# Optimization experiments

Hardware: AMD Instinct MI355X
Metric: run time of the kernel (lower is better)

Reference implementation:

```python
import jax, jax.numpy as jnp
import numpy as np

D = 128   # embedding_dim
H = 256   # hidden_dim

def setup_inputs() -> dict:
    key = jax.random.key(0)
    ks = jax.random.split(key, 16)
    s = 0.02
    B, N = 4, 384
    inp = {
        "cities": jax.random.uniform(ks[0], (B, N, 2), dtype=jnp.float32),
        # city_encoder: Linear(2,H) -> ReLU -> Linear(H,D); weights stored [in,out]
        "We1": jax.random.normal(ks[1], (2, H), dtype=jnp.float32) * s,
        "be1": jnp.zeros((H,), jnp.float32),
        "We2": jax.random.normal(ks[2], (H, D), dtype=jnp.float32) * s,
        "be2": jnp.zeros((D,), jnp.float32),
        # attention: Linear(D,H) -> ReLU -> Linear(H,1)
        "Wa1": jax.random.normal(ks[3], (D, H), dtype=jnp.float32) * s,
        "ba1": jnp.zeros((H,), jnp.float32),
        "wa2": jax.random.normal(ks[4], (H, 1), dtype=jnp.float32) * s,
        "ba2": jnp.zeros((1,), jnp.float32),
        # decoder: Linear(2D,H) -> ReLU -> Linear(H,1) -> Sigmoid
        "Wd1": jax.random.normal(ks[5], (2 * D, H), dtype=jnp.float32) * s,
        "bd1": jnp.zeros((H,), jnp.float32),
        "wd2": jax.random.normal(ks[6], (H, 1), dtype=jnp.float32) * s,
        "bd2": jnp.zeros((1,), jnp.float32),
    }
    return inp


def reference(cities, We1, be1, We2, be2, Wa1, ba1, wa2, ba2, Wd1, bd1, wd2, bd2):
    B, N, _ = cities.shape
    # city encoder MLP: [B,N,2] -> [B,N,D]
    emb = jax.nn.relu(cities @ We1 + be1) @ We2 + be2
    # attention scores -> softmax over cities
    att = jax.nn.softmax((jax.nn.relu(emb @ Wa1 + ba1) @ wa2 + ba2).squeeze(-1), axis=1)
    # Pairwise decoder: concat(e_i, e_j) @ Wd1 == e_i @ Wd1[:D] + e_j @ Wd1[D:]
    Ai = emb @ Wd1[:D]   # [B,N,H] contribution of row city i
    Aj = emb @ Wd1[D:]   # [B,N,H] contribution of col city j
    h = jax.nn.relu(Ai[:, :, None, :] + Aj[:, None, :, :] + bd1)  # [B,N,N,H]
    p = jax.nn.sigmoid((h @ wd2).squeeze(-1) + bd2)               # [B,N,N]
    # diagonal (i == j) was never written in the torch loop -> stays 0
    p = p * (1.0 - jnp.eye(N, dtype=p.dtype))
    return att, p
```

## Files before the change

### kernel.cpp

```cpp
#include <hip/hip_runtime.h>
#include <hip/hip_fp16.h>

#define NCITY 384
#define BATCH 4
#define DIM   128
#define HID   256
#define M_TOT (BATCH * NCITY)
#define TR    6

__device__ __forceinline__ void chunk_stream(
    const float* __restrict__ W,
    const float (*emb_s)[DIM], float* scr, int tid, float out6[TR])
{
    const int c4 = tid & 63;
    const int wv = tid >> 6;
    const int k0 = wv * 32;

    float4 acc[TR];
    #pragma unroll
    for (int rr = 0; rr < TR; ++rr) acc[rr] = make_float4(0.f, 0.f, 0.f, 0.f);

    #pragma unroll 2
    for (int kb = 0; kb < 32; kb += 4) {
        float4 ev[TR];
        #pragma unroll
        for (int rr = 0; rr < TR; ++rr)
            ev[rr] = *(const float4*)&emb_s[rr][k0 + kb];
        #pragma unroll
        for (int kk = 0; kk < 4; ++kk) {
            const float4 w4 = *(const float4*)&W[(k0 + kb + kk) * HID + c4 * 4];
            #pragma unroll
            for (int rr = 0; rr < TR; ++rr) {
                const float e = ((const float*)&ev[rr])[kk];
                acc[rr].x = fmaf(e, w4.x, acc[rr].x);
                acc[rr].y = fmaf(e, w4.y, acc[rr].y);
                acc[rr].z = fmaf(e, w4.z, acc[rr].z);
                acc[rr].w = fmaf(e, w4.w, acc[rr].w);
            }
        }
    }
    __syncthreads();
    #pragma unroll
    for (int rr = 0; rr < TR; ++rr)
        *(float4*)&scr[(wv * TR + rr) * HID + c4 * 4] = acc[rr];
    __syncthreads();
    #pragma unroll
    for (int rr = 0; rr < TR; ++rr)
        out6[rr] = scr[(0 * TR + rr) * HID + tid] + scr[(1 * TR + rr) * HID + tid]
                 + scr[(2 * TR + rr) * HID + tid] + scr[(3 * TR + rr) * HID + tid];
}

__global__ __launch_bounds__(256, 3) void encoder_stream(
    const float* __restrict__ cities,
    const float* __restrict__ We1, const float* __restrict__ be1,
    const float* __restrict__ We2, const float* __restrict__ be2,
    const float* __restrict__ Wa1, const float* __restrict__ ba1,
    const float* __restrict__ wa2, const float* __restrict__ ba2,
    const float* __restrict__ Wd1, const float* __restrict__ bd1,
    float* __restrict__ score, float* __restrict__ Ai, float* __restrict__ Aj)
{
    __shared__ float h1_s[TR][HID];
    __shared__ float emb_s[TR][DIM];
    __shared__ float scr[4 * TR * HID];
    __shared__ float red2[4][TR];

    const int tid = threadIdx.x;
    const int r0  = blockIdx.x * TR;

    {
        const float w0 = We1[tid], w1 = We1[HID + tid], b1v = be1[tid];
        #pragma unroll
        for (int rr = 0; rr < TR; ++rr) {
            const float cxx = cities[(r0 + rr) * 2];
            const float cyy = cities[(r0 + rr) * 2 + 1];
            h1_s[rr][tid] = fmaxf(fmaf(cxx, w0, fmaf(cyy, w1, b1v)), 0.f);
        }
    }
    __syncthreads();

    {
        const int d4 = tid & 31;
        const int k0 = (tid >> 5) * 32;
        float4 acc[TR];
        #pragma unroll
        for (int rr = 0; rr < TR; ++rr) acc[rr] = make_float4(0.f, 0.f, 0.f, 0.f);

        #pragma unroll 2
        for (int kb = 0; kb < 32; kb += 4) {
            float4 hv[TR];
            #pragma unroll
            for (int rr = 0; rr < TR; ++rr)
                hv[rr] = *(const float4*)&h1_s[rr][k0 + kb];
            #pragma unroll
            for (int kk = 0; kk < 4; ++kk) {
                const float4 w4 = *(const float4*)&We2[(k0 + kb + kk) * DIM + d4 * 4];
                #pragma unroll
                for (int rr = 0; rr < TR; ++rr) {
                    const float h = ((const float*)&hv[rr])[kk];
                    acc[rr].x = fmaf(h, w4.x, acc[rr].x);
                    acc[rr].y = fmaf(h, w4.y, acc[rr].y);
                    acc[rr].z = fmaf(h, w4.z, acc[rr].z);
                    acc[rr].w = fmaf(h, w4.w, acc[rr].w);
                }
            }
        }
        #pragma unroll
        for (int rr = 0; rr < TR; ++rr) {
            acc[rr].x += __shfl_xor(acc[rr].x, 32);
            acc[rr].y += __shfl_xor(acc[rr].y, 32);
            acc[rr].z += __shfl_xor(acc[rr].z, 32);
            acc[rr].w += __shfl_xor(acc[rr].w, 32);
        }
        if ((tid & 63) < 32) {
            const int wv = tid >> 6;
            #pragma unroll
            for (int rr = 0; rr < TR; ++rr)
                *(float4*)&scr[(wv * TR + rr) * DIM + d4 * 4] = acc[rr];
        }
        __syncthreads();
        for (int o = tid; o < TR * DIM; o += 256) {
            const int rr = o >> 7, d = o & (DIM - 1);
            emb_s[rr][d] = scr[(0 * TR + rr) * DIM + d] + scr[(1 * TR + rr) * DIM + d]
                         + scr[(2 * TR + rr) * DIM + d] + scr[(3 * TR + rr) * DIM + d]
                         + be2[d];
        }
        __syncthreads();
    }

    float o6[TR];

    chunk_stream(Wa1, emb_s, scr, tid, o6);
    {
        const float ba1v = ba1[tid], wa2v = wa2[tid];
        const int wv = tid >> 6;
        #pragma unroll
        for (int rr = 0; rr < TR; ++rr) {
            float v = fmaxf(o6[rr] + ba1v, 0.f) * wa2v;
            #pragma unroll
            for (int off = 32; off > 0; off >>= 1)
                v += __shfl_down(v, off);
            if ((tid & 63) == 0) red2[wv][rr] = v;
        }
        __syncthreads();
        if (tid < TR)
            score[r0 + tid] = red2[0][tid] + red2[1][tid] + red2[2][tid] + red2[3][tid];
    }

    chunk_stream(Wd1, emb_s, scr, tid, o6);
    {
        const float bd1v = bd1[tid];
        #pragma unroll
        for (int rr = 0; rr < TR; ++rr)
            Ai[(r0 + rr) * HID + tid] = o6[rr] + bd1v;
    }

    chunk_stream(Wd1 + DIM * HID, emb_s, scr, tid, o6);
    #pragma unroll
    for (int rr = 0; rr < TR; ++rr)
        Aj[(r0 + rr) * HID + tid] = o6[rr];
    (void)ba2;
}

__device__ __forceinline__ unsigned pk_add(unsigned a, unsigned b) {
    unsigned r; asm("v_pk_add_f16 %0, %1, %2" : "=v"(r) : "v"(a), "v"(b)); return r;
}
__device__ __forceinline__ unsigned pk_max0(unsigned a) {
    unsigned r; asm("v_pk_max_f16 %0, %1, %2" : "=v"(r) : "v"(a), "v"(0u)); return r;
}
__device__ __forceinline__ unsigned pk_fma(unsigned a, unsigned b, unsigned c) {
    unsigned r; asm("v_pk_fma_f16 %0, %1, %2, %3" : "=v"(r) : "v"(a), "v"(b), "v"(c)); return r;
}
__device__ __forceinline__ unsigned pack2(float a, float b) {
    union { __half2 h2; unsigned u; } c;
    c.h2 = __float22half2_rn(make_float2(a, b));
    return c.u;
}
__device__ __forceinline__ float sum2(unsigned u) {
    union { unsigned u; __half2 h2; } c; c.u = u;
    return __low2float(c.h2) + __high2float(c.h2);
}
union H8 { float4 f4; unsigned u[4]; };

__global__ __launch_bounds__(256) void pair_sm_kernel(
    const float* __restrict__ Ai, const float* __restrict__ Aj,
    const float* __restrict__ wd2, const float* __restrict__ bd2,
    const float* __restrict__ score, float* __restrict__ att,
    float* __restrict__ p)
{
    const int tid = threadIdx.x;
    const int b   = blockIdx.y;

    if (blockIdx.x == 144) {
        __shared__ float red[8];
        const int t = tid;
        const float v0 = score[b * NCITY + t];
        const bool  h2v = (t < NCITY - 256);
        const float v1 = h2v ? score[b * NCITY + 256 + t] : -3.4e38f;
        float m = fmaxf(v0, v1);
        #pragma unroll
        for (int off = 32; off > 0; off >>= 1)
            m = fmaxf(m, __shfl_down(m, off));
        if ((t & 63) == 0) red[t >> 6] = m;
        __syncthreads();
        m = fmaxf(fmaxf(red[0], red[1]), fmaxf(red[2], red[3]));
        const float e0 = __expf(v0 - m);
        const float e1 = h2v ? __expf(v1 - m) : 0.f;
        float s = e0 + e1;
        #pragma unroll
        for (int off = 32; off > 0; off >>= 1)
            s += __shfl_down(s, off);
        if ((t & 63) == 0) red[4 + (t >> 6)] = s;
        __syncthreads();
        s = red[4] + red[5] + red[6] + red[7];
        att[b * NCITY + t] = e0 / s;
        if (h2v) att[b * NCITY + 256 + t] = e1 / s;
        return;
    }

    __shared__ __half ai_s[32 * HID];
    __shared__ __half aj_s[32 * HID];
    __shared__ unsigned wd2h[HID / 2];

    const int i0 = (blockIdx.x / 12) * 32;
    const int j0 = (blockIdx.x % 12) * 32;

    if (tid < HID / 2) {
        const float2 w2 = *(const float2*)&wd2[tid * 2];
        wd2h[tid] = pack2(w2.x, w2.y);
    }

    for (int u = tid; u < 32 * 32; u += 256) {
        const int r = u >> 5, s = u & 31;
        const int su = (s ^ (r & 15)) * 8;
        {
            const int g = (b * NCITY + i0 + r) * HID + s * 8;
            const float4 f0 = *(const float4*)&Ai[g];
            const float4 f1 = *(const float4*)&Ai[g + 4];
            H8 pk;
            pk.u[0] = pack2(f0.x, f0.y);
            pk.u[1] = pack2(f0.z, f0.w);
            pk.u[2] = pack2(f1.x, f1.y);
            pk.u[3] = pack2(f1.z, f1.w);
            *(float4*)&ai_s[r * HID + su] = pk.f4;
        }
        {
            const int g = (b * NCITY + j0 + r) * HID + s * 8;
            const float4 f0 = *(const float4*)&Aj[g];
            const float4 f1 = *(const float4*)&Aj[g + 4];
            H8 pk;
            pk.u[0] = pack2(f0.x, f0.y);
            pk.u[1] = pack2(f0.z, f0.w);
            pk.u[2] = pack2(f1.x, f1.y);
            pk.u[3] = pack2(f1.z, f1.w);
            *(float4*)&aj_s[r * HID + su] = pk.f4;
        }
    }
    __syncthreads();

    const int tx = tid & 15;
    const int ty = tid >> 4;

    unsigned a00A = 0u, a00B = 0u, a01A = 0u, a01B = 0u;
    unsigned a10A = 0u, a10B = 0u, a11A = 0u, a11B = 0u;

    #pragma unroll 4
    for (int k8 = 0; k8 < 32; ++k8) {
        const int ci = (k8 ^ ty) * 8;
        const int cj = (k8 ^ tx) * 8;
        H8 x0, x1, y0, y1;
        x0.f4 = *(const float4*)&ai_s[ ty       * HID + ci];
        x1.f4 = *(const float4*)&ai_s[(ty + 16) * HID + ci];
        y0.f4 = *(const float4*)&aj_s[ tx       * HID + cj];
        y1.f4 = *(const float4*)&aj_s[(tx + 16) * HID + cj];

        #pragma unroll
        for (int q = 0; q < 4; ++q) {
            const unsigned w = wd2h[k8 * 4 + q];
            const unsigned t00 = pk_max0(pk_add(x0.u[q], y0.u[q]));
            const unsigned t01 = pk_max0(pk_add(x0.u[q], y1.u[q]));
            const unsigned t10 = pk_max0(pk_add(x1.u[q], y0.u[q]));
            const unsigned t11 = pk_max0(pk_add(x1.u[q], y1.u[q]));
            if (q < 2) {
                a00A = pk_fma(t00, w, a00A);
                a01A = pk_fma(t01, w, a01A);
                a10A = pk_fma(t10, w, a10A);
                a11A = pk_fma(t11, w, a11A);
            } else {
                a00B = pk_fma(t00, w, a00B);
                a01B = pk_fma(t01, w, a01B);
                a10B = pk_fma(t10, w, a10B);
                a11B = pk_fma(t11, w, a11B);
            }
        }
    }

    const float bd = bd2[0];
    float accs[2][2];
    accs[0][0] = sum2(a00A) + sum2(a00B);
    accs[0][1] = sum2(a01A) + sum2(a01B);
    accs[1][0] = sum2(a10A) + sum2(a10B);
    accs[1][1] = sum2(a11A) + sum2(a11B);

    #pragma unroll
    for (int ii = 0; ii < 2; ++ii) {
        #pragma unroll
        for (int jj = 0; jj < 2; ++jj) {
            const int gi = i0 + ty + ii * 16;
            const int gj = j0 + tx + jj * 16;
            const float v = 1.f / (1.f + __expf(-(accs[ii][jj] + bd)));
            p[(b * NCITY + gi) * NCITY + gj] = (gi == gj) ? 0.f : v;
        }
    }
}

extern "C" void kernel_launch(void* const* d_in, const int* in_sizes, int n_in,
                              void* d_out, int out_size, void* d_ws, size_t ws_size,
                              hipStream_t stream)
{
    const float* cities = (const float*)d_in[0];
    const float* We1    = (const float*)d_in[1];
    const float* be1    = (const float*)d_in[2];
    const float* We2    = (const float*)d_in[3];
    const float* be2    = (const float*)d_in[4];
    const float* Wa1    = (const float*)d_in[5];
    const float* ba1    = (const float*)d_in[6];
    const float* wa2    = (const float*)d_in[7];
    const float* ba2    = (const float*)d_in[8];
    const float* Wd1    = (const float*)d_in[9];
    const float* bd1    = (const float*)d_in[10];
    const float* wd2    = (const float*)d_in[11];
    const float* bd2    = (const float*)d_in[12];

    float* out_att = (float*)d_out;
    float* out_p   = out_att + M_TOT;

    float* score = (float*)d_ws;
    float* Ai    = score + M_TOT;
    float* Aj    = Ai + M_TOT * HID;

    encoder_stream<<<M_TOT / TR, 256, 0, stream>>>(
        cities, We1, be1, We2, be2, Wa1, ba1, wa2, ba2, Wd1, bd1,
        score, Ai, Aj);

    pair_sm_kernel<<<dim3(145, BATCH), 256, 0, stream>>>(
        Ai, Aj, wd2, bd2, score, out_att, out_p);
}
```

Measured before the change: 34.01 us.

## Fuse encoder and pairwise decoder into one persistent kernel with grid barrier

Merges the encoder and the pair/softmax kernels into a single launch of 256 blocks. A flag-based grid-wide barrier in global memory separates the two phases, and a persistent loop then distributes the 580 pair and softmax tasks over the blocks. Ai/Aj are now stored as fp16, which halves the intermediate traffic and removes the conversion step in the pair phase. This saves one kernel launch and its gap, but it relies on all 256 blocks being co-resident for the spin barrier and on the flags workspace starting in a consistent state.

```diff
diff --git a/kernel.cpp b/kernel.cpp
--- a/kernel.cpp
+++ b/kernel.cpp
@@ -7,6 +7,28 @@
 #define HID   256
 #define M_TOT (BATCH * NCITY)
 #define TR    6
+#define NBLK  (M_TOT / TR)
+#define NTASK (576 + BATCH)
+
+__device__ __forceinline__ unsigned pk_add(unsigned a, unsigned b) {
+    unsigned r; asm("v_pk_add_f16 %0, %1, %2" : "=v"(r) : "v"(a), "v"(b)); return r;
+}
+__device__ __forceinline__ unsigned pk_max0(unsigned a) {
+    unsigned r; asm("v_pk_max_f16 %0, %1, %2" : "=v"(r) : "v"(a), "v"(0u)); return r;
+}
+__device__ __forceinline__ unsigned pk_fma(unsigned a, unsigned b, unsigned c) {
+    unsigned r; asm("v_pk_fma_f16 %0, %1, %2, %3" : "=v"(r) : "v"(a), "v"(b), "v"(c)); return r;
+}
+__device__ __forceinline__ unsigned pack2(float a, float b) {
+    union { __half2 h2; unsigned u; } c;
+    c.h2 = __float22half2_rn(make_float2(a, b));
+    return c.u;
+}
+__device__ __forceinline__ float sum2(unsigned u) {
+    union { unsigned u; __half2 h2; } c; c.u = u;
+    return __low2float(c.h2) + __high2float(c.h2);
+}
+union H8 { float4 f4; unsigned u[4]; };
 
 __device__ __forceinline__ void chunk_stream(
     const float* __restrict__ W,
@@ -50,22 +72,29 @@
                  + scr[(2 * TR + rr) * HID + tid] + scr[(3 * TR + rr) * HID + tid];
 }
 
-__global__ __launch_bounds__(256, 3) void encoder_stream(
+__global__ __launch_bounds__(256) void fused_kernel(
     const float* __restrict__ cities,
     const float* __restrict__ We1, const float* __restrict__ be1,
     const float* __restrict__ We2, const float* __restrict__ be2,
     const float* __restrict__ Wa1, const float* __restrict__ ba1,
     const float* __restrict__ wa2, const float* __restrict__ ba2,
     const float* __restrict__ Wd1, const float* __restrict__ bd1,
-    float* __restrict__ score, float* __restrict__ Ai, float* __restrict__ Aj)
+    const float* __restrict__ wd2, const float* __restrict__ bd2,
+    float* __restrict__ score, __half* __restrict__ Ai_h, __half* __restrict__ Aj_h,
+    unsigned* __restrict__ flags,
+    float* __restrict__ att, float* __restrict__ p)
 {
-    __shared__ float h1_s[TR][HID];
-    __shared__ float emb_s[TR][DIM];
-    __shared__ float scr[4 * TR * HID];
-    __shared__ float red2[4][TR];
+    __shared__ float smem[8576];
+    __shared__ unsigned tgt_s;
+
+    float (*h1_s)[HID] = (float (*)[HID]) smem;
+    float (*emb_s)[DIM] = (float (*)[DIM])(smem + 1536);
+    float* red2 = smem + 2304;
+    float* scr  = smem + 2432;
 
     const int tid = threadIdx.x;
-    const int r0  = blockIdx.x * TR;
+    const int bid = blockIdx.x;
+    const int r0  = bid * TR;
 
     {
         const float w0 = We1[tid], w1 = We1[HID + tid], b1v = be1[tid];
@@ -139,11 +168,12 @@
             #pragma unroll
             for (int off = 32; off > 0; off >>= 1)
                 v += __shfl_down(v, off);
-            if ((tid & 63) == 0) red2[wv][rr] = v;
+            if ((tid & 63) == 0) red2[wv * TR + rr] = v;
         }
         __syncthreads();
         if (tid < TR)
-            score[r0 + tid] = red2[0][tid] + red2[1][tid] + red2[2][tid] + red2[3][tid];
+            score[r0 + tid] = red2[0 * TR + tid] + red2[1 * TR + tid]
+                            + red2[2 * TR + tid] + red2[3 * TR + tid];
     }
 
     chunk_stream(Wd1, emb_s, scr, tid, o6);
@@ -151,164 +181,137 @@
         const float bd1v = bd1[tid];
         #pragma unroll
         for (int rr = 0; rr < TR; ++rr)
-            Ai[(r0 + rr) * HID + tid] = o6[rr] + bd1v;
+            Ai_h[(r0 + rr) * HID + tid] = __float2half(o6[rr] + bd1v);
     }
 
     chunk_stream(Wd1 + DIM * HID, emb_s, scr, tid, o6);
     #pragma unroll
     for (int rr = 0; rr < TR; ++rr)
-        Aj[(r0 + rr) * HID + tid] = o6[rr];
+        Aj_h[(r0 + rr) * HID + tid] = __float2half(o6[rr]);
     (void)ba2;
-}
-
-__device__ __forceinline__ unsigned pk_add(unsigned a, unsigned b) {
-    unsigned r; asm("v_pk_add_f16 %0, %1, %2" : "=v"(r) : "v"(a), "v"(b)); return r;
-}
-__device__ __forceinline__ unsigned pk_max0(unsigned a) {
-    unsigned r; asm("v_pk_max_f16 %0, %1, %2" : "=v"(r) : "v"(a), "v"(0u)); return r;
-}
-__device__ __forceinline__ unsigned pk_fma(unsigned a, unsigned b, unsigned c) {
-    unsigned r; asm("v_pk_fma_f16 %0, %1, %2, %3" : "=v"(r) : "v"(a), "v"(b), "v"(c)); return r;
-}
-__device__ __forceinline__ unsigned pack2(float a, float b) {
-    union { __half2 h2; unsigned u; } c;
-    c.h2 = __float22half2_rn(make_float2(a, b));
-    return c.u;
-}
-__device__ __forceinline__ float sum2(unsigned u) {
-    union { unsigned u; __half2 h2; } c; c.u = u;
-    return __low2float(c.h2) + __high2float(c.h2);
-}
-union H8 { float4 f4; unsigned u[4]; };
-
-__global__ __launch_bounds__(256) void pair_sm_kernel(
-    const float* __restrict__ Ai, const float* __restrict__ Aj,
-    const float* __restrict__ wd2, const float* __restrict__ bd2,
-    const float* __restrict__ score, float* __restrict__ att,
-    float* __restrict__ p)
-{
-    const int tid = threadIdx.x;
-    const int b   = blockIdx.y;
-
-    if (blockIdx.x == 144) {
-        __shared__ float red[8];
-        const int t = tid;
-        const float v0 = score[b * NCITY + t];
-        const bool  h2v = (t < NCITY - 256);
-        const float v1 = h2v ? score[b * NCITY + 256 + t] : -3.4e38f;
-        float m = fmaxf(v0, v1);
-        #pragma unroll
-        for (int off = 32; off > 0; off >>= 1)
-            m = fmaxf(m, __shfl_down(m, off));
-        if ((t & 63) == 0) red[t >> 6] = m;
+
+    __threadfence();
+    __syncthreads();
+    if (tid == 0) {
+        const unsigned oldv = __hip_atomic_load(&flags[bid], __ATOMIC_RELAXED,
+                                                __HIP_MEMORY_SCOPE_AGENT);
+        tgt_s = oldv + 1u;
+        __hip_atomic_store(&flags[bid], oldv + 1u, __ATOMIC_RELEASE,
+                           __HIP_MEMORY_SCOPE_AGENT);
+    }
+    __syncthreads();
+    {
+        const unsigned target = tgt_s;
+        while (__hip_atomic_load(&flags[tid], __ATOMIC_RELAXED,
+                                 __HIP_MEMORY_SCOPE_AGENT) != target) {}
+    }
+    __threadfence();
+    __syncthreads();
+
+    const float bd = bd2[0];
+    __half*   ai_s = (__half*)smem;
+    __half*   aj_s = (__half*)smem + 32 * HID;
+    unsigned* wd2h = (unsigned*)(smem + 8192);
+    float*    redm = smem + 8320;
+
+    for (int t = bid; t < NTASK; t += NBLK) {
         __syncthreads();
-        m = fmaxf(fmaxf(red[0], red[1]), fmaxf(red[2], red[3]));
-        const float e0 = __expf(v0 - m);
-        const float e1 = h2v ? __expf(v1 - m) : 0.f;
-        float s = e0 + e1;
-        #pragma unroll
-        for (int off = 32; off > 0; off >>= 1)
-            s += __shfl_down(s, off);
-        if ((t & 63) == 0) red[4 + (t >> 6)] = s;
-        __syncthreads();
-        s = red[4] + red[5] + red[6] + red[7];
-        att[b * NCITY + t] = e0 / s;
-        if (h2v) att[b * NCITY + 256 + t] = e1 / s;
-        return;
-    }
-
-    __shared__ __half ai_s[32 * HID];
-    __shared__ __half aj_s[32 * HID];
-    __shared__ unsigned wd2h[HID / 2];
-
-    const int i0 = (blockIdx.x / 12) * 32;
-    const int j0 = (blockIdx.x % 12) * 32;
-
-    if (tid < HID / 2) {
-        const float2 w2 = *(const float2*)&wd2[tid * 2];
-        wd2h[tid] = pack2(w2.x, w2.y);
-    }
-
-    for (int u = tid; u < 32 * 32; u += 256) {
-        const int r = u >> 5, s = u & 31;
-        const int su = (s ^ (r & 15)) * 8;
-        {
-            const int g = (b * NCITY + i0 + r) * HID + s * 8;
-            const float4 f0 = *(const float4*)&Ai[g];
-            const float4 f1 = *(const float4*)&Ai[g + 4];
-            H8 pk;
-            pk.u[0] = pack2(f0.x, f0.y);
-            pk.u[1] = pack2(f0.z, f0.w);
-            pk.u[2] = pack2(f1.x, f1.y);
-            pk.u[3] = pack2(f1.z, f1.w);
-            *(float4*)&ai_s[r * HID + su] = pk.f4;
-        }
-        {
-            const int g = (b * NCITY + j0 + r) * HID + s * 8;
-            const float4 f0 = *(const float4*)&Aj[g];
-            const float4 f1 = *(const float4*)&Aj[g + 4];
-            H8 pk;
-            pk.u[0] = pack2(f0.x, f0.y);
-            pk.u[1] = pack2(f0.z, f0.w);
-            pk.u[2] = pack2(f1.x, f1.y);
-            pk.u[3] = pack2(f1.z, f1.w);
-            *(float4*)&aj_s[r * HID + su] = pk.f4;
-        }
-    }
-    __syncthreads();
-
-    const int tx = tid & 15;
-    const int ty = tid >> 4;
-
-    unsigned a00A = 0u, a00B = 0u, a01A = 0u, a01B = 0u;
-    unsigned a10A = 0u, a10B = 0u, a11A = 0u, a11B = 0u;
-
-    #pragma unroll 4
-    for (int k8 = 0; k8 < 32; ++k8) {
-        const int ci = (k8 ^ ty) * 8;
-        const int cj = (k8 ^ tx) * 8;
-        H8 x0, x1, y0, y1;
-        x0.f4 = *(const float4*)&ai_s[ ty       * HID + ci];
-        x1.f4 = *(const float4*)&ai_s[(ty + 16) * HID + ci];
-        y0.f4 = *(const float4*)&aj_s[ tx       * HID + cj];
-        y1.f4 = *(const float4*)&aj_s[(tx + 16) * HID + cj];
-
-        #pragma unroll
-        for (int q = 0; q < 4; ++q) {
-            const unsigned w = wd2h[k8 * 4 + q];
-            const unsigned t00 = pk_max0(pk_add(x0.u[q], y0.u[q]));
-            const unsigned t01 = pk_max0(pk_add(x0.u[q], y1.u[q]));
-            const unsigned t10 = pk_max0(pk_add(x1.u[q], y0.u[q]));
-            const unsigned t11 = pk_max0(pk_add(x1.u[q], y1.u[q]));
-            if (q < 2) {
-                a00A = pk_fma(t00, w, a00A);
-                a01A = pk_fma(t01, w, a01A);
-                a10A = pk_fma(t10, w, a10A);
-                a11A = pk_fma(t11, w, a11A);
-            } else {
-                a00B = pk_fma(t00, w, a00B);
-                a01B = pk_fma(t01, w, a01B);
-                a10B = pk_fma(t10, w, a10B);
-                a11B = pk_fma(t11, w, a11B);
-            }
-        }
-    }
-
-    const float bd = bd2[0];
-    float accs[2][2];
-    accs[0][0] = sum2(a00A) + sum2(a00B);
-    accs[0][1] = sum2(a01A) + sum2(a01B);
-    accs[1][0] = sum2(a10A) + sum2(a10B);
-    accs[1][1] = sum2(a11A) + sum2(a11B);
-
-    #pragma unroll
-    for (int ii = 0; ii < 2; ++ii) {
-        #pragma unroll
-        for (int jj = 0; jj < 2; ++jj) {
-            const int gi = i0 + ty + ii * 16;
-            const int gj = j0 + tx + jj * 16;
-            const float v = 1.f / (1.f + __expf(-(accs[ii][jj] + bd)));
-            p[(b * NCITY + gi) * NCITY + gj] = (gi == gj) ? 0.f : v;
+        if (t < 576) {
+            const int b   = t / 144;
+            const int rem = t % 144;
+            const int i0  = (rem / 12) * 32;
+            const int j0  = (rem % 12) * 32;
+
+            if (tid < HID / 2) {
+                const float2 w2 = *(const float2*)&wd2[tid * 2];
+                wd2h[tid] = pack2(w2.x, w2.y);
+            }
+            for (int u = tid; u < 32 * 32; u += 256) {
+                const int r = u >> 5, s = u & 31;
+                const int su = (s ^ (r & 15)) * 8;
+                *(float4*)&ai_s[r * HID + su] =
+                    *(const float4*)&Ai_h[(b * NCITY + i0 + r) * HID + s * 8];
+                *(float4*)&aj_s[r * HID + su] =
+                    *(const float4*)&Aj_h[(b * NCITY + j0 + r) * HID + s * 8];
+            }
+            __syncthreads();
+
+            const int tx = tid & 15;
+            const int ty = tid >> 4;
+
+            unsigned a00A = 0u, a00B = 0u, a01A = 0u, a01B = 0u;
+            unsigned a10A = 0u, a10B = 0u, a11A = 0u, a11B = 0u;
+
+            #pragma unroll 4
+            for (int k8 = 0; k8 < 32; ++k8) {
+                const int ci = (k8 ^ ty) * 8;
+                const int cj = (k8 ^ tx) * 8;
+                H8 x0, x1, y0, y1;
+                x0.f4 = *(const float4*)&ai_s[ ty       * HID + ci];
+                x1.f4 = *(const float4*)&ai_s[(ty + 16) * HID + ci];
+                y0.f4 = *(const float4*)&aj_s[ tx       * HID + cj];
+                y1.f4 = *(const float4*)&aj_s[(tx + 16) * HID + cj];
+
+                #pragma unroll
+                for (int q = 0; q < 4; ++q) {
+                    const unsigned w = wd2h[k8 * 4 + q];
+                    const unsigned t00 = pk_max0(pk_add(x0.u[q], y0.u[q]));
+                    const unsigned t01 = pk_max0(pk_add(x0.u[q], y1.u[q]));
+                    const unsigned t10 = pk_max0(pk_add(x1.u[q], y0.u[q]));
+                    const unsigned t11 = pk_max0(pk_add(x1.u[q], y1.u[q]));
+                    if (q < 2) {
+                        a00A = pk_fma(t00, w, a00A);
+                        a01A = pk_fma(t01, w, a01A);
+                        a10A = pk_fma(t10, w, a10A);
+                        a11A = pk_fma(t11, w, a11A);
+                    } else {
+                        a00B = pk_fma(t00, w, a00B);
+                        a01B = pk_fma(t01, w, a01B);
+                        a10B = pk_fma(t10, w, a10B);
+                        a11B = pk_fma(t11, w, a11B);
+                    }
+                }
+            }
+
+            float accs[2][2];
+            accs[0][0] = sum2(a00A) + sum2(a00B);
+            accs[0][1] = sum2(a01A) + sum2(a01B);
+            accs[1][0] = sum2(a10A) + sum2(a10B);
+            accs[1][1] = sum2(a11A) + sum2(a11B);
+
+            #pragma unroll
+            for (int ii = 0; ii < 2; ++ii) {
+                #pragma unroll
+                for (int jj = 0; jj < 2; ++jj) {
+                    const int gi = i0 + ty + ii * 16;
+                    const int gj = j0 + tx + jj * 16;
+                    const float v = 1.f / (1.f + __expf(-(accs[ii][jj] + bd)));
+                    p[(b * NCITY + gi) * NCITY + gj] = (gi == gj) ? 0.f : v;
+                }
+            }
+        } else {
+            const int bb = t - 576;
+            const float v0 = score[bb * NCITY + tid];
+            const bool  h2v = (tid < NCITY - 256);
+            const float v1 = h2v ? score[bb * NCITY + 256 + tid] : -3.4e38f;
+            float m = fmaxf(v0, v1);
+            #pragma unroll
+            for (int off = 32; off > 0; off >>= 1)
+                m = fmaxf(m, __shfl_down(m, off));
+            if ((tid & 63) == 0) redm[tid >> 6] = m;
+            __syncthreads();
+            m = fmaxf(fmaxf(redm[0], redm[1]), fmaxf(redm[2], redm[3]));
+            const float e0 = __expf(v0 - m);
+            const float e1 = h2v ? __expf(v1 - m) : 0.f;
+            float s = e0 + e1;
+            #pragma unroll
+            for (int off = 32; off > 0; off >>= 1)
+                s += __shfl_down(s, off);
+            if ((tid & 63) == 0) redm[4 + (tid >> 6)] = s;
+            __syncthreads();
+            s = redm[4] + redm[5] + redm[6] + redm[7];
+            att[bb * NCITY + tid] = e0 / s;
+            if (h2v) att[bb * NCITY + 256 + tid] = e1 / s;
         }
     }
 }
@@ -334,14 +337,12 @@
     float* out_att = (float*)d_out;
     float* out_p   = out_att + M_TOT;
 
-    float* score = (float*)d_ws;
-    float* Ai    = score + M_TOT;
-    float* Aj    = Ai + M_TOT * HID;
-
-    encoder_stream<<<M_TOT / TR, 256, 0, stream>>>(
-        cities, We1, be1, We2, be2, Wa1, ba1, wa2, ba2, Wd1, bd1,
-        score, Ai, Aj);
-
-    pair_sm_kernel<<<dim3(145, BATCH), 256, 0, stream>>>(
-        Ai, Aj, wd2, bd2, score, out_att, out_p);
-}
+    float*    score = (float*)d_ws;
+    __half*   Ai_h  = (__half*)(score + M_TOT);
+    __half*   Aj_h  = Ai_h + M_TOT * HID;
+    unsigned* flags = (unsigned*)(Aj_h + M_TOT * HID);
+
+    fused_kernel<<<NBLK, 256, 0, stream>>>(
+        cities, We1, be1, We2, be2, Wa1, ba1, wa2, ba2, Wd1, bd1, wd2, bd2,
+        score, Ai_h, Aj_h, flags, out_att, out_p);
+}
```

Result: slower. 79.67 us (+134.3%).

## Split encoder into fp16 weight conversion, embedding, and tiled packed-fp16 head GEMM kernels

Applied to the files above, without the earlier changes.

The monolithic encoder kernel is replaced by a pipeline. A convert kernel packs We2, Wa1 and Wd1 to fp16, an embedding kernel writes fp16 embeddings, and a heads kernel runs a 64x128-tiled GEMM with v_pk_fma_f16 over the concatenated head weights. The heads kernel writes Ai/Aj directly in fp16 plus partial attention scores, so the pair kernel no longer converts on load. This gives much better weight reuse than streaming the weights per 6 rows, but adds two kernel launches and accumulates the head GEMMs in fp16, which costs precision.

```diff
diff --git a/kernel.cpp b/kernel.cpp
--- a/kernel.cpp
+++ b/kernel.cpp
@@ -5,64 +5,67 @@
 #define BATCH 4
 #define DIM   128
 #define HID   256
-#define M_TOT (BATCH * NCITY)
+#define M_TOT 1536
 #define TR    6
 
-__device__ __forceinline__ void chunk_stream(
-    const float* __restrict__ W,
-    const float (*emb_s)[DIM], float* scr, int tid, float out6[TR])
+typedef unsigned short u16;
+
+__device__ __forceinline__ unsigned pk_add(unsigned a, unsigned b) {
+    unsigned r; asm("v_pk_add_f16 %0, %1, %2" : "=v"(r) : "v"(a), "v"(b)); return r;
+}
+__device__ __forceinline__ unsigned pk_max0(unsigned a) {
+    unsigned r; asm("v_pk_max_f16 %0, %1, %2" : "=v"(r) : "v"(a), "v"(0u)); return r;
+}
+__device__ __forceinline__ unsigned pk_fma(unsigned a, unsigned b, unsigned c) {
+    unsigned r; asm("v_pk_fma_f16 %0, %1, %2, %3" : "=v"(r) : "v"(a), "v"(b), "v"(c)); return r;
+}
+__device__ __forceinline__ unsigned pack2(float a, float b) {
+    union { __half2 h2; unsigned u; } c;
+    c.h2 = __float22half2_rn(make_float2(a, b));
+    return c.u;
+}
+__device__ __forceinline__ float sum2(unsigned u) {
+    union { unsigned u; __half2 h2; } c; c.u = u;
+    return __low2float(c.h2) + __high2float(c.h2);
+}
+__device__ __forceinline__ u16 h_bits(float x) {
+    union { __half h; u16 s; } c;
+    c.h = __float2half(x);
+    return c.s;
+}
+union H8 { float4 f4; unsigned u[4]; };
+
+__global__ __launch_bounds__(256) void convert_kernel(
+    const float* __restrict__ We2, const float* __restrict__ Wa1,
+    const float* __restrict__ Wd1,
+    unsigned* __restrict__ We2h_u, unsigned* __restrict__ Wh_u)
 {
-    const int c4 = tid & 63;
-    const int wv = tid >> 6;
-    const int k0 = wv * 32;
-
-    float4 acc[TR];
-    #pragma unroll
-    for (int rr = 0; rr < TR; ++rr) acc[rr] = make_float4(0.f, 0.f, 0.f, 0.f);
-
-    #pragma unroll 2
-    for (int kb = 0; kb < 32; kb += 4) {
-        float4 ev[TR];
-        #pragma unroll
-        for (int rr = 0; rr < TR; ++rr)
-            ev[rr] = *(const float4*)&emb_s[rr][k0 + kb];
-        #pragma unroll
-        for (int kk = 0; kk < 4; ++kk) {
-            const float4 w4 = *(const float4*)&W[(k0 + kb + kk) * HID + c4 * 4];
-            #pragma unroll
-            for (int rr = 0; rr < TR; ++rr) {
-                const float e = ((const float*)&ev[rr])[kk];
-                acc[rr].x = fmaf(e, w4.x, acc[rr].x);
-                acc[rr].y = fmaf(e, w4.y, acc[rr].y);
-                acc[rr].z = fmaf(e, w4.z, acc[rr].z);
-                acc[rr].w = fmaf(e, w4.w, acc[rr].w);
-            }
-        }
-    }
-    __syncthreads();
-    #pragma unroll
-    for (int rr = 0; rr < TR; ++rr)
-        *(float4*)&scr[(wv * TR + rr) * HID + c4 * 4] = acc[rr];
-    __syncthreads();
-    #pragma unroll
-    for (int rr = 0; rr < TR; ++rr)
-        out6[rr] = scr[(0 * TR + rr) * HID + tid] + scr[(1 * TR + rr) * HID + tid]
-                 + scr[(2 * TR + rr) * HID + tid] + scr[(3 * TR + rr) * HID + tid];
-}
-
-__global__ __launch_bounds__(256, 3) void encoder_stream(
+    const int i = blockIdx.x * 256 + threadIdx.x;
+    if (i < 16384) {
+        const float2 f = *(const float2*)&We2[2 * i];
+        We2h_u[i] = pack2(f.x, f.y);
+    } else {
+        const int j = i - 16384;
+        const int k = j / 384;
+        const int t = j - k * 384;
+        const int n = 2 * t;
+        const float* src;
+        if (n < 256)      src = &Wa1[k * 256 + n];
+        else if (n < 512) src = &Wd1[k * 256 + (n - 256)];
+        else              src = &Wd1[(128 + k) * 256 + (n - 512)];
+        const float2 f = *(const float2*)src;
+        Wh_u[j] = pack2(f.x, f.y);
+    }
+}
+
+__global__ __launch_bounds__(256) void emb_kernel(
     const float* __restrict__ cities,
     const float* __restrict__ We1, const float* __restrict__ be1,
-    const float* __restrict__ We2, const float* __restrict__ be2,
-    const float* __restrict__ Wa1, const float* __restrict__ ba1,
-    const float* __restrict__ wa2, const float* __restrict__ ba2,
-    const float* __restrict__ Wd1, const float* __restrict__ bd1,
-    float* __restrict__ score, float* __restrict__ Ai, float* __restrict__ Aj)
+    const u16* __restrict__ We2h, const float* __restrict__ be2,
+    u16* __restrict__ emb_h)
 {
     __shared__ float h1_s[TR][HID];
-    __shared__ float emb_s[TR][DIM];
-    __shared__ float scr[4 * TR * HID];
-    __shared__ float red2[4][TR];
+    __shared__ float scr[4 * TR * DIM];
 
     const int tid = threadIdx.x;
     const int r0  = blockIdx.x * TR;
@@ -78,113 +81,183 @@
     }
     __syncthreads();
 
+    const int d4 = tid & 31;
+    const int k0 = (tid >> 5) * 32;
+    float4 acc[TR];
+    #pragma unroll
+    for (int rr = 0; rr < TR; ++rr) acc[rr] = make_float4(0.f, 0.f, 0.f, 0.f);
+
+    #pragma unroll 2
+    for (int kb = 0; kb < 32; kb += 4) {
+        float4 hv[TR];
+        #pragma unroll
+        for (int rr = 0; rr < TR; ++rr)
+            hv[rr] = *(const float4*)&h1_s[rr][k0 + kb];
+        #pragma unroll
+        for (int kk = 0; kk < 4; ++kk) {
+            const u16* wp = &We2h[(k0 + kb + kk) * DIM + d4 * 4];
+            const float2 w01 = __half22float2(*(const __half2*)wp);
+            const float2 w23 = __half22float2(*(const __half2*)(wp + 2));
+            #pragma unroll
+            for (int rr = 0; rr < TR; ++rr) {
+                const float h = ((const float*)&hv[rr])[kk];
+                acc[rr].x = fmaf(h, w01.x, acc[rr].x);
+                acc[rr].y = fmaf(h, w01.y, acc[rr].y);
+                acc[rr].z = fmaf(h, w23.x, acc[rr].z);
+                acc[rr].w = fmaf(h, w23.y, acc[rr].w);
+            }
+        }
+    }
+    #pragma unroll
+    for (int rr = 0; rr < TR; ++rr) {
+        acc[rr].x += __shfl_xor(acc[rr].x, 32);
+        acc[rr].y += __shfl_xor(acc[rr].y, 32);
+        acc[rr].z += __shfl_xor(acc[rr].z, 32);
+        acc[rr].w += __shfl_xor(acc[rr].w, 32);
+    }
+    if ((tid & 63) < 32) {
+        const int wv = tid >> 6;
+        #pragma unroll
+        for (int rr = 0; rr < TR; ++rr)
+            *(float4*)&scr[(wv * TR + rr) * DIM + d4 * 4] = acc[rr];
+    }
+    __syncthreads();
+    #pragma unroll
+    for (int j = 0; j < 3; ++j) {
+        const int o = tid + j * 256;
+        const int rr = o >> 7, d = o & (DIM - 1);
+        const float v = scr[(0 * TR + rr) * DIM + d] + scr[(1 * TR + rr) * DIM + d]
+                      + scr[(2 * TR + rr) * DIM + d] + scr[(3 * TR + rr) * DIM + d]
+                      + be2[d];
+        emb_h[(r0 + rr) * DIM + d] = h_bits(v);
+    }
+}
+
+__global__ __launch_bounds__(256) void heads_kernel(
+    const u16* __restrict__ emb_h, const u16* __restrict__ Wh,
+    const float* __restrict__ ba1, const float* __restrict__ wa2,
+    const float* __restrict__ bd1,
+    float* __restrict__ score_part,
+    u16* __restrict__ Ai_u, u16* __restrict__ Aj_u)
+{
+    __shared__ unsigned lds_a[64 * 64];
+    __shared__ unsigned lds_b[64 * 128];
+
+    const int tid = threadIdx.x;
+    const int g   = blockIdx.x;
+    const int r0  = blockIdx.y * 64;
+    const int n0  = g * 128;
+
     {
-        const int d4 = tid & 31;
-        const int k0 = (tid >> 5) * 32;
-        float4 acc[TR];
-        #pragma unroll
-        for (int rr = 0; rr < TR; ++rr) acc[rr] = make_float4(0.f, 0.f, 0.f, 0.f);
-
-        #pragma unroll 2
-        for (int kb = 0; kb < 32; kb += 4) {
-            float4 hv[TR];
+        const int r = tid & 63, dg = tid >> 6;
+        #pragma unroll
+        for (int v = 0; v < 4; ++v) {
+            const uint4 q = *(const uint4*)&emb_h[(r0 + r) * DIM + dg * 32 + v * 8];
+            const int d2 = dg * 16 + v * 4;
+            lds_a[(d2 + 0) * 64 + r] = q.x;
+            lds_a[(d2 + 1) * 64 + r] = q.y;
+            lds_a[(d2 + 2) * 64 + r] = q.z;
+            lds_a[(d2 + 3) * 64 + r] = q.w;
+        }
+    }
+    {
+        const int c8 = tid & 15, k2g = tid >> 4;
+        #pragma unroll
+        for (int v = 0; v < 4; ++v) {
+            const int k2 = k2g * 4 + v;
+            const uint4 q0 = *(const uint4*)&Wh[(2 * k2)     * 768 + n0 + c8 * 8];
+            const uint4 q1 = *(const uint4*)&Wh[(2 * k2 + 1) * 768 + n0 + c8 * 8];
+            uint4 lo, hi;
+            lo.x = (q0.x & 0xffffu) | (q1.x << 16);
+            lo.y = (q0.x >> 16)     | (q1.x & 0xffff0000u);
+            lo.z = (q0.y & 0xffffu) | (q1.y << 16);
+            lo.w = (q0.y >> 16)     | (q1.y & 0xffff0000u);
+            hi.x = (q0.z & 0xffffu) | (q1.z << 16);
+            hi.y = (q0.z >> 16)     | (q1.z & 0xffff0000u);
+            hi.z = (q0.w & 0xffffu) | (q1.w << 16);
+            hi.w = (q0.w >> 16)     | (q1.w & 0xffff0000u);
+            *(uint4*)&lds_b[k2 * 128 + c8 * 8]     = lo;
+            *(uint4*)&lds_b[k2 * 128 + c8 * 8 + 4] = hi;
+        }
+    }
+    __syncthreads();
+
+    const int tx = tid & 15;
+    const int ty = tid >> 4;
+    unsigned acc[4][8] = {};
+
+    #pragma unroll 4
+    for (int k2 = 0; k2 < 64; ++k2) {
+        const uint4 a  = *(const uint4*)&lds_a[k2 * 64 + ty * 4];
+        const uint4 b0 = *(const uint4*)&lds_b[k2 * 128 + tx * 8];
+        const uint4 b1 = *(const uint4*)&lds_b[k2 * 128 + tx * 8 + 4];
+        const unsigned aa[4] = {a.x, a.y, a.z, a.w};
+        const unsigned bb[8] = {b0.x, b0.y, b0.z, b0.w, b1.x, b1.y, b1.z, b1.w};
+        #pragma unroll
+        for (int i = 0; i < 4; ++i)
             #pragma unroll
-            for (int rr = 0; rr < TR; ++rr)
-                hv[rr] = *(const float4*)&h1_s[rr][k0 + kb];
+            for (int j = 0; j < 8; ++j)
+                acc[i][j] = pk_fma(aa[i], bb[j], acc[i][j]);
+    }
+
+    float out[4][8];
+    #pragma unroll
+    for (int i = 0; i < 4; ++i)
+        #pragma unroll
+        for (int j = 0; j < 8; ++j)
+            out[i][j] = sum2(acc[i][j]);
+
+    if (g < 2) {
+        float ba[8], wa[8];
+        *(float4*)&ba[0] = *(const float4*)&ba1[n0 + tx * 8];
+        *(float4*)&ba[4] = *(const float4*)&ba1[n0 + tx * 8 + 4];
+        *(float4*)&wa[0] = *(const float4*)&wa2[n0 + tx * 8];
+        *(float4*)&wa[4] = *(const float4*)&wa2[n0 + tx * 8 + 4];
+        #pragma unroll
+        for (int i = 0; i < 4; ++i) {
+            float s = 0.f;
             #pragma unroll
-            for (int kk = 0; kk < 4; ++kk) {
-                const float4 w4 = *(const float4*)&We2[(k0 + kb + kk) * DIM + d4 * 4];
-                #pragma unroll
-                for (int rr = 0; rr < TR; ++rr) {
-                    const float h = ((const float*)&hv[rr])[kk];
-                    acc[rr].x = fmaf(h, w4.x, acc[rr].x);
-                    acc[rr].y = fmaf(h, w4.y, acc[rr].y);
-                    acc[rr].z = fmaf(h, w4.z, acc[rr].z);
-                    acc[rr].w = fmaf(h, w4.w, acc[rr].w);
-                }
-            }
-        }
-        #pragma unroll
-        for (int rr = 0; rr < TR; ++rr) {
-            acc[rr].x += __shfl_xor(acc[rr].x, 32);
-            acc[rr].y += __shfl_xor(acc[rr].y, 32);
-            acc[rr].z += __shfl_xor(acc[rr].z, 32);
-            acc[rr].w += __shfl_xor(acc[rr].w, 32);
-        }
-        if ((tid & 63) < 32) {
-            const int wv = tid >> 6;
-            #pragma unroll
-            for (int rr = 0; rr < TR; ++rr)
-                *(float4*)&scr[(wv * TR + rr) * DIM + d4 * 4] = acc[rr];
-        }
-        __syncthreads();
-        for (int o = tid; o < TR * DIM; o += 256) {
-            const int rr = o >> 7, d = o & (DIM - 1);
-            emb_s[rr][d] = scr[(0 * TR + rr) * DIM + d] + scr[(1 * TR + rr) * DIM + d]
-                         + scr[(2 * TR + rr) * DIM + d] + scr[(3 * TR + rr) * DIM + d]
-                         + be2[d];
-        }
-        __syncthreads();
-    }
-
-    float o6[TR];
-
-    chunk_stream(Wa1, emb_s, scr, tid, o6);
-    {
-        const float ba1v = ba1[tid], wa2v = wa2[tid];
-        const int wv = tid >> 6;
-        #pragma unroll
-        for (int rr = 0; rr < TR; ++rr) {
-            float v = fmaxf(o6[rr] + ba1v, 0.f) * wa2v;
-            #pragma unroll
-            for (int off = 32; off > 0; off >>= 1)
-                v += __shfl_down(v, off);
-            if ((tid & 63) == 0) red2[wv][rr] = v;
-        }
-        __syncthreads();
-        if (tid < TR)
-            score[r0 + tid] = red2[0][tid] + red2[1][tid] + red2[2][tid] + red2[3][tid];
-    }
-
-    chunk_stream(Wd1, emb_s, scr, tid, o6);
-    {
-        const float bd1v = bd1[tid];
-        #pragma unroll
-        for (int rr = 0; rr < TR; ++rr)
-            Ai[(r0 + rr) * HID + tid] = o6[rr] + bd1v;
-    }
-
-    chunk_stream(Wd1 + DIM * HID, emb_s, scr, tid, o6);
-    #pragma unroll
-    for (int rr = 0; rr < TR; ++rr)
-        Aj[(r0 + rr) * HID + tid] = o6[rr];
-    (void)ba2;
-}
-
-__device__ __forceinline__ unsigned pk_add(unsigned a, unsigned b) {
-    unsigned r; asm("v_pk_add_f16 %0, %1, %2" : "=v"(r) : "v"(a), "v"(b)); return r;
-}
-__device__ __forceinline__ unsigned pk_max0(unsigned a) {
-    unsigned r; asm("v_pk_max_f16 %0, %1, %2" : "=v"(r) : "v"(a), "v"(0u)); return r;
-}
-__device__ __forceinline__ unsigned pk_fma(unsigned a, unsigned b, unsigned c) {
-    unsigned r; asm("v_pk_fma_f16 %0, %1, %2, %3" : "=v"(r) : "v"(a), "v"(b), "v"(c)); return r;
-}
-__device__ __forceinline__ unsigned pack2(float a, float b) {
-    union { __half2 h2; unsigned u; } c;
-    c.h2 = __float22half2_rn(make_float2(a, b));
-    return c.u;
-}
-__device__ __forceinline__ float sum2(unsigned u) {
-    union { unsigned u; __half2 h2; } c; c.u = u;
-    return __low2float(c.h2) + __high2float(c.h2);
-}
-union H8 { float4 f4; unsigned u[4]; };
+            for (int j = 0; j < 8; ++j)
+                s += fmaxf(out[i][j] + ba[j], 0.f) * wa[j];
+            s += __shfl_xor(s, 1);
+            s += __shfl_xor(s, 2);
+            s += __shfl_xor(s, 4);
+            s += __shfl_xor(s, 8);
+            if (tx == 0)
+                score_part[g * M_TOT + r0 + ty * 4 + i] = s;
+        }
+    } else if (g < 4) {
+        const int c0 = (g - 2) * 128 + tx * 8;
+        float bd[8];
+        *(float4*)&bd[0] = *(const float4*)&bd1[c0];
+        *(float4*)&bd[4] = *(const float4*)&bd1[c0 + 4];
+        #pragma unroll
+        for (int i = 0; i < 4; ++i) {
+            uint4 o;
+            o.x = (unsigned)h_bits(out[i][0] + bd[0]) | ((unsigned)h_bits(out[i][1] + bd[1]) << 16);
+            o.y = (unsigned)h_bits(out[i][2] + bd[2]) | ((unsigned)h_bits(out[i][3] + bd[3]) << 16);
+            o.z = (unsigned)h_bits(out[i][4] + bd[4]) | ((unsigned)h_bits(out[i][5] + bd[5]) << 16);
+            o.w = (unsigned)h_bits(out[i][6] + bd[6]) | ((unsigned)h_bits(out[i][7] + bd[7]) << 16);
+            *(uint4*)&Ai_u[(r0 + ty * 4 + i) * HID + c0] = o;
+        }
+    } else {
+        const int c0 = (g - 4) * 128 + tx * 8;
+        #pragma unroll
+        for (int i = 0; i < 4; ++i) {
+            uint4 o;
+            o.x = (unsigned)h_bits(out[i][0]) | ((unsigned)h_bits(out[i][1]) << 16);
+            o.y = (unsigned)h_bits(out[i][2]) | ((unsigned)h_bits(out[i][3]) << 16);
+            o.z = (unsigned)h_bits(out[i][4]) | ((unsigned)h_bits(out[i][5]) << 16);
+            o.w = (unsigned)h_bits(out[i][6]) | ((unsigned)h_bits(out[i][7]) << 16);
+            *(uint4*)&Aj_u[(r0 + ty * 4 + i) * HID + c0] = o;
+        }
+    }
+}
 
 __global__ __launch_bounds__(256) void pair_sm_kernel(
-    const float* __restrict__ Ai, const float* __restrict__ Aj,
+    const __half* __restrict__ Ai, const __half* __restrict__ Aj,
     const float* __restrict__ wd2, const float* __restrict__ bd2,
-    const float* __restrict__ score, float* __restrict__ att,
+    const float* __restrict__ sp, float* __restrict__ att,
     float* __restrict__ p)
 {
     const int tid = threadIdx.x;
@@ -193,9 +266,10 @@
     if (blockIdx.x == 144) {
         __shared__ float red[8];
         const int t = tid;
-        const float v0 = score[b * NCITY + t];
+        const float v0 = sp[b * NCITY + t] + sp[M_TOT + b * NCITY + t];
         const bool  h2v = (t < NCITY - 256);
-        const float v1 = h2v ? score[b * NCITY + 256 + t] : -3.4e38f;
+        const float v1 = h2v ? (sp[b * NCITY + 256 + t] + sp[M_TOT + b * NCITY + 256 + t])
+                             : -3.4e38f;
         float m = fmaxf(v0, v1);
         #pragma unroll
         for (int off = 32; off > 0; off >>= 1)
@@ -232,28 +306,10 @@
     for (int u = tid; u < 32 * 32; u += 256) {
         const int r = u >> 5, s = u & 31;
         const int su = (s ^ (r & 15)) * 8;
-        {
-            const int g = (b * NCITY + i0 + r) * HID + s * 8;
-            const float4 f0 = *(const float4*)&Ai[g];
-            const float4 f1 = *(const float4*)&Ai[g + 4];
-            H8 pk;
-            pk.u[0] = pack2(f0.x, f0.y);
-            pk.u[1] = pack2(f0.z, f0.w);
-            pk.u[2] = pack2(f1.x, f1.y);
-            pk.u[3] = pack2(f1.z, f1.w);
-            *(float4*)&ai_s[r * HID + su] = pk.f4;
-        }
-        {
-            const int g = (b * NCITY + j0 + r) * HID + s * 8;
-            const float4 f0 = *(const float4*)&Aj[g];
-            const float4 f1 = *(const float4*)&Aj[g + 4];
-            H8 pk;
-            pk.u[0] = pack2(f0.x, f0.y);
-            pk.u[1] = pack2(f0.z, f0.w);
-            pk.u[2] = pack2(f1.x, f1.y);
-            pk.u[3] = pack2(f1.z, f1.w);
-            *(float4*)&aj_s[r * HID + su] = pk.f4;
-        }
+        *(float4*)&ai_s[r * HID + su] =
+            *(const float4*)&Ai[(b * NCITY + i0 + r) * HID + s * 8];
+        *(float4*)&aj_s[r * HID + su] =
+            *(const float4*)&Aj[(b * NCITY + j0 + r) * HID + s * 8];
     }
     __syncthreads();
 
@@ -330,18 +386,27 @@
     const float* bd1    = (const float*)d_in[10];
     const float* wd2    = (const float*)d_in[11];
     const float* bd2    = (const float*)d_in[12];
+    (void)ba2;
 
     float* out_att = (float*)d_out;
     float* out_p   = out_att + M_TOT;
 
-    float* score = (float*)d_ws;
-    float* Ai    = score + M_TOT;
-    float* Aj    = Ai + M_TOT * HID;
-
-    encoder_stream<<<M_TOT / TR, 256, 0, stream>>>(
-        cities, We1, be1, We2, be2, Wa1, ba1, wa2, ba2, Wd1, bd1,
-        score, Ai, Aj);
+    float*    score_part = (float*)d_ws;
+    unsigned* We2h_u = (unsigned*)(score_part + 2 * M_TOT);
+    unsigned* Wh_u   = We2h_u + 16384;
+    u16*      emb_h  = (u16*)(Wh_u + 49152);
+    u16*      Ai_u   = emb_h + M_TOT * DIM;
+    u16*      Aj_u   = Ai_u + M_TOT * HID;
+
+    convert_kernel<<<256, 256, 0, stream>>>(We2, Wa1, Wd1, We2h_u, Wh_u);
+
+    emb_kernel<<<256, 256, 0, stream>>>(
+        cities, We1, be1, (const u16*)We2h_u, be2, emb_h);
+
+    heads_kernel<<<dim3(6, 24), 256, 0, stream>>>(
+        emb_h, (const u16*)Wh_u, ba1, wa2, bd1, score_part, Ai_u, Aj_u);
 
     pair_sm_kernel<<<dim3(145, BATCH), 256, 0, stream>>>(
-        Ai, Aj, wd2, bd2, score, out_att, out_p);
-}
+        (const __half*)Ai_u, (const __half*)Aj_u, wd2, bd2,
+        score_part, out_att, out_p);
+}
```

New measurement: 39.65 us. +16.6%, slower.
